# Kernel tuning notes

Hardware: AMD Instinct MI355X
Metric: run time of the kernel (lower is better)

## Reference

```python
import jax, jax.numpy as jnp
import numpy as np

EPS = 1e-5
NEG_SLOPE = 0.2

def _conv1x1(x, w):
    # x: (B,C,N,K), w: (O,C) -> (B,O,N,K)
    return jnp.einsum('oc,bcnk->bonk', w, x)

def _bn(x, g, b, m, v):
    scale = g / jnp.sqrt(v + EPS)
    return x * scale[None, :, None, None] + (b - m * scale)[None, :, None, None]

def _lrelu(x):
    return jnp.where(x > 0, x, NEG_SLOPE * x)

def setup_inputs() -> dict:
    key = jax.random.key(0)
    specs = {
        'x': ((8, 6, 8192, 20), 'randn'),
        'trans_w': ((64, 6), 'randn'), 'trans_g': ((64,), 'rand'), 'trans_b': ((64,), 'randn'),
        'trans_m': ((64,), 'randn'), 'trans_v': ((64,), 'rand'),
        'pos_w1': ((64, 3), 'randn'), 'pos_g': ((64,), 'rand'), 'pos_b': ((64,), 'randn'),
        'pos_m': ((64,), 'randn'), 'pos_v': ((64,), 'rand'),
        'pos_w2': ((64, 64), 'randn'), 'pos_b2': ((64,), 'randn'),
        'gate_w1': ((16, 6), 'randn'), 'gate_g': ((16,), 'rand'), 'gate_b': ((16,), 'randn'),
        'gate_m': ((16,), 'randn'), 'gate_v': ((16,), 'rand'),
        'gate_w2': ((1, 16), 'randn'), 'gate_b2': ((1,), 'ones'),
        'attn_w1': ((16, 6), 'randn'), 'attn_g': ((16,), 'rand'), 'attn_b': ((16,), 'randn'),
        'attn_m': ((16,), 'randn'), 'attn_v': ((16,), 'rand'),
        'attn_w2': ((64, 16), 'randn'), 'attn_b2': ((64,), 'randn'),
    }
    out = {}
    for i, (name, (shape, fill)) in enumerate(specs.items()):
        k = jax.random.fold_in(key, i)
        if fill == 'randn':
            out[name] = jax.random.normal(k, shape, dtype=jnp.float32) * 0.1
        elif fill == 'rand':
            out[name] = jax.random.uniform(k, shape, dtype=jnp.float32)
        else:  # ones (gate bias init to 2.0 in original; scale ones)
            out[name] = jnp.ones(shape, dtype=jnp.float32) * 2.0
    return out

def reference(x, trans_w, trans_g, trans_b, trans_m, trans_v,
              pos_w1, pos_g, pos_b, pos_m, pos_v, pos_w2, pos_b2,
              gate_w1, gate_g, gate_b, gate_m, gate_v, gate_w2, gate_b2,
              attn_w1, attn_g, attn_b, attn_m, attn_v, attn_w2, attn_b2):
    in_channels = 3
    rel_pos = x[:, in_channels:in_channels + 3, :, :]  # (B,3,N,K)
    # pos_net: conv(3->C) + BN + LReLU + conv(C->C, bias)
    pos_h = _lrelu(_bn(_conv1x1(rel_pos, pos_w1), pos_g, pos_b, pos_m, pos_v))
    pos_enc = _conv1x1(pos_h, pos_w2) + pos_b2[None, :, None, None]
    # trans: conv(2*Cin->C) + BN + LReLU
    trans_feat = _lrelu(_bn(_conv1x1(x, trans_w), trans_g, trans_b, trans_m, trans_v)) + pos_enc
    # gate_net: conv(6->16)+BN+LReLU+conv(16->1,bias)+sigmoid (dropout=0 in eval)
    gate_h = _lrelu(_bn(_conv1x1(x, gate_w1), gate_g, gate_b, gate_m, gate_v))
    gate_map = jax.nn.sigmoid(_conv1x1(gate_h, gate_w2) + gate_b2[None, :, None, None])  # (B,1,N,K)
    clean_feat = trans_feat * gate_map
    # attn_net: conv(6->16)+BN+LReLU+conv(16->C,bias), then + pos_enc, softmax over K
    attn_h = _lrelu(_bn(_conv1x1(x, attn_w1), attn_g, attn_b, attn_m, attn_v))
    attn_logits = _conv1x1(attn_h, attn_w2) + attn_b2[None, :, None, None] + pos_enc
    attn_weights = jax.nn.softmax(attn_logits, axis=-1)
    out_attn = (trans_feat * attn_weights).sum(axis=-1)  # (B,C,N)
    out_max = clean_feat.max(axis=-1)                    # (B,C,N)
    return out_attn + out_max
```

## Files before the change

### kernel.cpp

```cpp
#include <hip/hip_runtime.h>
#include <math.h>

#define NEG 0.2f
#define EPSV 1e-5f

typedef _Float16 v8h __attribute__((ext_vector_type(8)));
typedef _Float16 v4h __attribute__((ext_vector_type(4)));
typedef _Float16 v2h __attribute__((ext_vector_type(2)));
typedef __fp16   f16x2 __attribute__((ext_vector_type(2)));
typedef float    v4f __attribute__((ext_vector_type(4)));

__device__ __forceinline__ float lrelu(float v) { return fmaxf(v, NEG * v); }
__device__ __forceinline__ v4f lrelu4(v4f v) {
    return __builtin_elementwise_max(v, v * NEG);
}
__device__ __forceinline__ v2h lreluh2(v2h v) {
    return __builtin_elementwise_max(v, v * (_Float16)NEG);
}

__device__ __forceinline__ v2h pk(float a, float b) {
    union { f16x2 i; v2h o; } u;
    u.i = __builtin_amdgcn_cvt_pkrtz(a, b);
    return u.o;
}

#define MFMA32(a, b, c) __builtin_amdgcn_mfma_f32_16x16x32_f16((a), (b), (c), 0, 0, 0)
#define MFMA16(a, b, c) __builtin_amdgcn_mfma_f32_16x16x16f16((a), (b), (c), 0, 0, 0)

__global__ __launch_bounds__(256, 4)
void gsl_mfma(const float* __restrict__ x,
              const float* __restrict__ trans_w, const float* __restrict__ trans_g,
              const float* __restrict__ trans_b, const float* __restrict__ trans_m,
              const float* __restrict__ trans_v,
              const float* __restrict__ pos_w1, const float* __restrict__ pos_g,
              const float* __restrict__ pos_b, const float* __restrict__ pos_m,
              const float* __restrict__ pos_v, const float* __restrict__ pos_w2,
              const float* __restrict__ pos_b2,
              const float* __restrict__ gate_w1, const float* __restrict__ gate_g,
              const float* __restrict__ gate_b, const float* __restrict__ gate_m,
              const float* __restrict__ gate_v, const float* __restrict__ gate_w2,
              const float* __restrict__ gate_b2,
              const float* __restrict__ attn_w1, const float* __restrict__ attn_g,
              const float* __restrict__ attn_b, const float* __restrict__ attn_m,
              const float* __restrict__ attn_v, const float* __restrict__ attn_w2,
              const float* __restrict__ attn_b2,
              float* __restrict__ out)
{
    __shared__ _Float16 WHL[1536];
    __shared__ _Float16 W2L[4096];
    __shared__ float    PB2[64];

    const int tid  = threadIdx.x;
    const int wv   = tid >> 6;
    const int lane = tid & 63;
    const int p    = lane & 15;
    const int q    = lane >> 4;

    const int b  = blockIdx.x >> 7;
    const int n0 = ((blockIdx.x & 127) << 6) | (wv << 4);
    const int n  = n0 | p;

    #pragma unroll
    for (int e = 0; e < 16; ++e) {
        int idx = tid * 16 + e;
        int t   = idx >> 9;
        int rem = idx & 511;
        int l   = rem >> 3;
        int j   = rem & 7;
        int qk  = l >> 4;
        int pp  = l & 15;
        int hl  = (j < 4) ? (4 * qk + j) : (16 + 4 * qk + (j - 4));
        W2L[t * 512 + l * 8 + j] =
            (_Float16)pos_w2[((t >> 1) * 16 + pp) * 64 + (t & 1) * 32 + hl];
    }

    if (tid < 64) {
        const int c = tid;
        float sp = pos_g[c] * rsqrtf(pos_v[c] + EPSV);
        float bp = pos_b[c] - pos_m[c] * sp;
        const int mt = c >> 4, pp = c & 15;
        for (int k = 0; k < 16; ++k) {
            float v = (k >= 3 && k < 6) ? pos_w1[c * 3 + (k - 3)] * sp
                                        : ((k == 6) ? bp : 0.f);
            WHL[mt * 256 + ((k >> 2) * 16 + pp) * 4 + (k & 3)] = (_Float16)v;
        }
        PB2[c] = pos_b2[c];
    } else if (tid < 80) {
        const int j = tid - 64;
        float sa = attn_g[j] * rsqrtf(attn_v[j] + EPSV);
        float ba = attn_b[j] - attn_m[j] * sa;
        for (int k = 0; k < 16; ++k) {
            float v = (k < 6) ? attn_w1[j * 6 + k] * sa : ((k == 6) ? ba : 0.f);
            WHL[1024 + ((k >> 2) * 16 + j) * 4 + (k & 3)] = (_Float16)v;
        }
    } else if (tid < 96) {
        const int j = tid - 80;
        float sg = gate_g[j] * rsqrtf(gate_v[j] + EPSV);
        float bg = gate_b[j] - gate_m[j] * sg;
        for (int k = 0; k < 16; ++k) {
            float v = (k < 6) ? gate_w1[j * 6 + k] * sg : ((k == 6) ? bg : 0.f);
            WHL[1280 + ((k >> 2) * 16 + j) * 4 + (k & 3)] = (_Float16)v;
        }
    }

    v4h WTf[4], WA2f[4], WG2f;
    #pragma unroll
    for (int mt = 0; mt < 4; ++mt) {
        const int ch = mt * 16 + p;
        #pragma unroll
        for (int i = 0; i < 4; ++i)
            WA2f[mt][i] = (_Float16)attn_w2[ch * 16 + q * 4 + i];
        float st = trans_g[ch] * rsqrtf(trans_v[ch] + EPSV);
        float bt = trans_b[ch] - trans_m[ch] * st;
        #pragma unroll
        for (int i = 0; i < 4; ++i) {
            int k = q * 4 + i;
            float v = (k < 6) ? trans_w[ch * 6 + k] * st : ((k == 6) ? bt : 0.f);
            WTf[mt][i] = (_Float16)v;
        }
    }
    #pragma unroll
    for (int i = 0; i < 4; ++i)
        WG2f[i] = (_Float16)gate_w2[4 * q + i];
    const float gb2v = gate_b2[0];

    __syncthreads();

    const _Float16* const WHLp = WHL + lane * 4;
    const _Float16* const W2Lp = W2L + lane * 8;
    const float* const    PB2p = PB2 + 4 * q;

    const v4f zero = {0.f, 0.f, 0.f, 0.f};
    v4f den[4], num[4], cmx[4];
    #pragma unroll
    for (int mt = 0; mt < 4; ++mt) {
        den[mt] = zero; num[mt] = zero;
        cmx[mt] = (v4f){-3.4e38f, -3.4e38f, -3.4e38f, -3.4e38f};
    }

    const float* xb = x + ((size_t)(b * 6) * 8192 + n) * 20;
    const int hi = q & 1;
    const float* const s0p = xb + (size_t)(hi ? 4 : 0) * 163840;
    const float* const s1p = xb + (size_t)(hi ? 5 : 1) * 163840;
    const float* const s2p = xb + (size_t)(hi ? 4 : 2) * 163840;
    const float* const s3p = xb + (size_t)(hi ? 5 : 3) * 163840;

    auto mk = [&](float a, float bb, float cc, float dd) -> v4h {
        v2h lo = pk(a, bb);
        v2h hh = pk(cc, dd);
        if (hi) { union { unsigned u; v2h h; } t; t.u = 0x00003C00u; hh = t.h; }
        return (v4h){lo.x, lo.y, hh.x, hh.y};
    };

    float c0 = s0p[0], c1 = s1p[0], c2 = s2p[0], c3 = s3p[0];

    #pragma unroll 1
    for (int k = 0; k < 20; ++k) {
        asm volatile("" ::: "memory");

        v4h xv = mk(c0, c1, c2, c3);
        if (k < 19) {
            c0 = s0p[k + 1]; c1 = s1p[k + 1];
            c2 = s2p[k + 1]; c3 = s3p[k + 1];
        }

        union { v8h v; v4h h[2]; } uA, uC;
        #pragma unroll
        for (int mt = 0; mt < 4; ++mt) {
            v4f php = MFMA16(*(const v4h*)(WHLp + mt * 256), xv, zero);
            v2h e0 = lreluh2(pk(php[0], php[1]));
            v2h e1 = lreluh2(pk(php[2], php[3]));
            v4h pkd = (v4h){e0.x, e0.y, e1.x, e1.y};
            if (mt < 2) uA.h[mt] = pkd; else uC.h[mt - 2] = pkd;
        }
        v4f ahp = MFMA16(*(const v4h*)(WHLp + 1024), xv, zero);
        union { v4h v; v2h h[2]; } ua;
        ua.h[0] = lreluh2(pk(ahp[0], ahp[1]));
        ua.h[1] = lreluh2(pk(ahp[2], ahp[3]));
        const v4h ahB = ua.v;

        v4f ghp = MFMA16(*(const v4h*)(WHLp + 1280), xv, zero);
        union { v4h v; v2h h[2]; } ug;
        ug.h[0] = lreluh2(pk(ghp[0], ghp[1]));
        ug.h[1] = lreluh2(pk(ghp[2], ghp[3]));
        v4f gav = MFMA16(WG2f, ug.v, zero);
        const float gate = 1.f / (1.f + __expf(-(gav[0] + gb2v)));

        #pragma unroll
        for (int mt = 0; mt < 4; ++mt) {
            v8h w2a = *(const v8h*)(W2Lp + (mt * 2 + 0) * 512);
            v8h w2b = *(const v8h*)(W2Lp + (mt * 2 + 1) * 512);
            v4f pe = MFMA32(w2a, uA.v, *(const v4f*)(PB2p + mt * 16));
            pe = MFMA32(w2b, uC.v, pe);
            v4f tfa = MFMA16(WTf[mt], xv, zero);
            v4f tfv = lrelu4(tfa) + pe;
            pe = MFMA16(WA2f[mt], ahB, pe);
            v4f e;
            #pragma unroll
            for (int r = 0; r < 4; ++r) e[r] = __expf(pe[r]);
            den[mt] += e;
            num[mt] += tfv * e;
            cmx[mt] = __builtin_elementwise_max(cmx[mt], tfv * gate);
        }
    }

    #pragma unroll
    for (int mt = 0; mt < 4; ++mt) {
        #pragma unroll
        for (int r = 0; r < 4; ++r) {
            const int ch = mt * 16 + 4 * q + r;
            out[((size_t)(b * 64 + ch)) * 8192 + n] =
                num[mt][r] / den[mt][r] + cmx[mt][r];
        }
    }
}

extern "C" void kernel_launch(void* const* d_in, const int* in_sizes, int n_in,
                              void* d_out, int out_size, void* d_ws, size_t ws_size,
                              hipStream_t stream) {
    const float* x       = (const float*)d_in[0];
    const float* trans_w = (const float*)d_in[1];
    const float* trans_g = (const float*)d_in[2];
    const float* trans_b = (const float*)d_in[3];
    const float* trans_m = (const float*)d_in[4];
    const float* trans_v = (const float*)d_in[5];
    const float* pos_w1  = (const float*)d_in[6];
    const float* pos_g   = (const float*)d_in[7];
    const float* pos_b   = (const float*)d_in[8];
    const float* pos_m   = (const float*)d_in[9];
    const float* pos_v   = (const float*)d_in[10];
    const float* pos_w2  = (const float*)d_in[11];
    const float* pos_b2  = (const float*)d_in[12];
    const float* gate_w1 = (const float*)d_in[13];
    const float* gate_g  = (const float*)d_in[14];
    const float* gate_b  = (const float*)d_in[15];
    const float* gate_m  = (const float*)d_in[16];
    const float* gate_v  = (const float*)d_in[17];
    const float* gate_w2 = (const float*)d_in[18];
    const float* gate_b2 = (const float*)d_in[19];
    const float* attn_w1 = (const float*)d_in[20];
    const float* attn_g  = (const float*)d_in[21];
    const float* attn_b  = (const float*)d_in[22];
    const float* attn_m  = (const float*)d_in[23];
    const float* attn_v  = (const float*)d_in[24];
    const float* attn_w2 = (const float*)d_in[25];
    const float* attn_b2 = (const float*)d_in[26];
    float* out = (float*)d_out;

    gsl_mfma<<<1024, 256, 0, stream>>>(
        x, trans_w, trans_g, trans_b, trans_m, trans_v,
        pos_w1, pos_g, pos_b, pos_m, pos_v, pos_w2, pos_b2,
        gate_w1, gate_g, gate_b, gate_m, gate_v, gate_w2, gate_b2,
        attn_w1, attn_g, attn_b, attn_m, attn_v, attn_w2, attn_b2,
        out);
}
```

Measured before the change: 170.5 us.

## Split output channels across wave pairs and double grid size

```diff
diff --git a/kernel.cpp b/kernel.cpp
--- a/kernel.cpp
+++ b/kernel.cpp
@@ -27,7 +27,7 @@
 #define MFMA32(a, b, c) __builtin_amdgcn_mfma_f32_16x16x32_f16((a), (b), (c), 0, 0, 0)
 #define MFMA16(a, b, c) __builtin_amdgcn_mfma_f32_16x16x16f16((a), (b), (c), 0, 0, 0)
 
-__global__ __launch_bounds__(256, 4)
+__global__ __launch_bounds__(256, 6)
 void gsl_mfma(const float* __restrict__ x,
               const float* __restrict__ trans_w, const float* __restrict__ trans_g,
               const float* __restrict__ trans_b, const float* __restrict__ trans_m,
@@ -56,8 +56,12 @@
     const int p    = lane & 15;
     const int q    = lane >> 4;
 
-    const int b  = blockIdx.x >> 7;
-    const int n0 = ((blockIdx.x & 127) << 6) | (wv << 4);
+    const int pw  = wv & 1;
+    const int mh  = wv >> 1;
+    const int mtb = mh * 2;
+
+    const int b  = blockIdx.x >> 8;
+    const int n0 = ((blockIdx.x & 255) << 5) | (pw << 4);
     const int n  = n0 | p;
 
     #pragma unroll
@@ -103,20 +107,20 @@
         }
     }
 
-    v4h WTf[4], WA2f[4], WG2f;
-    #pragma unroll
-    for (int mt = 0; mt < 4; ++mt) {
-        const int ch = mt * 16 + p;
+    v4h WTf[2], WA2f[2], WG2f;
+    #pragma unroll
+    for (int t = 0; t < 2; ++t) {
+        const int ch = (mtb + t) * 16 + p;
         #pragma unroll
         for (int i = 0; i < 4; ++i)
-            WA2f[mt][i] = (_Float16)attn_w2[ch * 16 + q * 4 + i];
+            WA2f[t][i] = (_Float16)attn_w2[ch * 16 + q * 4 + i];
         float st = trans_g[ch] * rsqrtf(trans_v[ch] + EPSV);
         float bt = trans_b[ch] - trans_m[ch] * st;
         #pragma unroll
         for (int i = 0; i < 4; ++i) {
             int k = q * 4 + i;
             float v = (k < 6) ? trans_w[ch * 6 + k] * st : ((k == 6) ? bt : 0.f);
-            WTf[mt][i] = (_Float16)v;
+            WTf[t][i] = (_Float16)v;
         }
     }
     #pragma unroll
@@ -131,11 +135,11 @@
     const float* const    PB2p = PB2 + 4 * q;
 
     const v4f zero = {0.f, 0.f, 0.f, 0.f};
-    v4f den[4], num[4], cmx[4];
-    #pragma unroll
-    for (int mt = 0; mt < 4; ++mt) {
-        den[mt] = zero; num[mt] = zero;
-        cmx[mt] = (v4f){-3.4e38f, -3.4e38f, -3.4e38f, -3.4e38f};
+    v4f den[2], num[2], cmx[2];
+    #pragma unroll
+    for (int t = 0; t < 2; ++t) {
+        den[t] = zero; num[t] = zero;
+        cmx[t] = (v4f){-3.4e38f, -3.4e38f, -3.4e38f, -3.4e38f};
     }
 
     const float* xb = x + ((size_t)(b * 6) * 8192 + n) * 20;
@@ -187,30 +191,31 @@
         const float gate = 1.f / (1.f + __expf(-(gav[0] + gb2v)));
 
         #pragma unroll
-        for (int mt = 0; mt < 4; ++mt) {
+        for (int t = 0; t < 2; ++t) {
+            const int mt = mtb + t;
             v8h w2a = *(const v8h*)(W2Lp + (mt * 2 + 0) * 512);
             v8h w2b = *(const v8h*)(W2Lp + (mt * 2 + 1) * 512);
             v4f pe = MFMA32(w2a, uA.v, *(const v4f*)(PB2p + mt * 16));
             pe = MFMA32(w2b, uC.v, pe);
-            v4f tfa = MFMA16(WTf[mt], xv, zero);
+            v4f tfa = MFMA16(WTf[t], xv, zero);
             v4f tfv = lrelu4(tfa) + pe;
-            pe = MFMA16(WA2f[mt], ahB, pe);
+            pe = MFMA16(WA2f[t], ahB, pe);
             v4f e;
             #pragma unroll
             for (int r = 0; r < 4; ++r) e[r] = __expf(pe[r]);
-            den[mt] += e;
-            num[mt] += tfv * e;
-            cmx[mt] = __builtin_elementwise_max(cmx[mt], tfv * gate);
-        }
-    }
-
-    #pragma unroll
-    for (int mt = 0; mt < 4; ++mt) {
+            den[t] += e;
+            num[t] += tfv * e;
+            cmx[t] = __builtin_elementwise_max(cmx[t], tfv * gate);
+        }
+    }
+
+    #pragma unroll
+    for (int t = 0; t < 2; ++t) {
         #pragma unroll
         for (int r = 0; r < 4; ++r) {
-            const int ch = mt * 16 + 4 * q + r;
+            const int ch = (mtb + t) * 16 + 4 * q + r;
             out[((size_t)(b * 64 + ch)) * 8192 + n] =
-                num[mt][r] / den[mt][r] + cmx[mt][r];
+                num[t][r] / den[t][r] + cmx[t][r];
         }
     }
 }
@@ -247,7 +252,7 @@
     const float* attn_b2 = (const float*)d_in[26];
     float* out = (float*)d_out;
 
-    gsl_mfma<<<1024, 256, 0, stream>>>(
+    gsl_mfma<<<2048, 256, 0, stream>>>(
         x, trans_w, trans_g, trans_b, trans_m, trans_v,
         pos_w1, pos_g, pos_b, pos_m, pos_v, pos_w2, pos_b2,
         gate_w1, gate_g, gate_b, gate_m, gate_v, gate_w2, gate_b2,
```

Result: slower. 184.6 us (+8.3%).
